# Kernel tuning notes

Hardware: AMD Instinct MI355X
Metric: run time of the kernel (lower is better)

The kernel has to match this reference:

```python
import jax, jax.numpy as jnp
import numpy as np

K = 3
PAD = 1


def conv2d(x, w, b, pad):
    y = jax.lax.conv_general_dilated(
        x, w, window_strides=(1, 1), padding=[(pad, pad), (pad, pad)],
        dimension_numbers=("NCHW", "OIHW", "NCHW"))
    return y + b[None, :, None, None]


def dcn_v2(f, w_off, b_off, w, b):
    # Modulated deformable conv (DCNv2), stride=1, pad=1, dilation=1, dg=1.
    B, C, H, W = f.shape
    om = conv2d(f, w_off, b_off, PAD)                 # [B, 27, H, W]
    o1, o2, m = jnp.split(om, 3, axis=1)
    offset = jnp.concatenate([o1, o2], axis=1).reshape(B, K * K, 2, H, W)
    dy, dx = offset[:, :, 0], offset[:, :, 1]          # [B, 9, H, W]
    mask = jax.nn.sigmoid(m)                           # [B, 9, H, W]
    ky = (jnp.arange(K * K) // K).astype(f.dtype)      # kernel row per tap
    kx = (jnp.arange(K * K) % K).astype(f.dtype)       # kernel col per tap
    hh = jnp.arange(H, dtype=f.dtype)
    ww = jnp.arange(W, dtype=f.dtype)
    ys = hh[None, None, :, None] - PAD + ky[None, :, None, None] + dy  # [B,9,H,W]
    xs = ww[None, None, None, :] - PAD + kx[None, :, None, None] + dx
    y0 = jnp.floor(ys)
    x0 = jnp.floor(xs)
    wy1 = ys - y0
    wx1 = xs - x0
    wy0 = 1.0 - wy1
    wx0 = 1.0 - wx1
    f_flat = f.reshape(B, C, H * W)

    def gather(yi, xi):
        valid = (yi >= 0) & (yi <= H - 1) & (xi >= 0) & (xi <= W - 1)
        yc = jnp.clip(yi, 0, H - 1).astype(jnp.int32)
        xc = jnp.clip(xi, 0, W - 1).astype(jnp.int32)
        idx = (yc * W + xc).reshape(B, 1, -1)          # [B,1,9*H*W]
        g = jnp.take_along_axis(f_flat, idx, axis=2).reshape(B, C, K * K, H, W)
        return g * valid.astype(f.dtype).reshape(B, 1, K * K, H, W)

    v = (gather(y0, x0) * (wy0 * wx0)[:, None]
         + gather(y0, x0 + 1) * (wy0 * wx1)[:, None]
         + gather(y0 + 1, x0) * (wy1 * wx0)[:, None]
         + gather(y0 + 1, x0 + 1) * (wy1 * wx1)[:, None])   # [B,C,9,H,W]
    v = v * mask[:, None]
    out = jnp.einsum("bckhw,ock->bohw", v, w.reshape(w.shape[0], C, K * K))
    return out + b[None, :, None, None]


def setup_inputs() -> dict:
    key = jax.random.key(0)
    ks = jax.random.split(key, 10)
    B, C, H, W = 2, 256, 128, 128
    s = 0.05
    return {
        "x": jax.random.normal(ks[0], (B, C, H, W), jnp.float32),
        "votes": jax.random.normal(ks[1], (B, C, H, W), jnp.float32),
        "w1": jax.random.normal(ks[2], (C, C, 3, 3), jnp.float32) * s,
        "b1": jnp.zeros((C,), jnp.float32),
        "w_off": jax.random.normal(ks[3], (27, C, 3, 3), jnp.float32) * 0.01,
        "b_off": jnp.zeros((27,), jnp.float32),
        "w_dcn": jax.random.normal(ks[4], (C, C, 3, 3), jnp.float32) * s,
        "b_dcn": jnp.zeros((C,), jnp.float32),
        "w2": jax.random.normal(ks[5], (C, C, 3, 3), jnp.float32) * s,
        "b2": jnp.zeros((C,), jnp.float32),
        "w3": jax.random.normal(ks[6], (C, C, 3, 3), jnp.float32) * s,
        "b3": jnp.zeros((C,), jnp.float32),
        "w4": jax.random.normal(ks[7], (2, C, 1, 1), jnp.float32) * s,
        "b4": jnp.zeros((2,), jnp.float32),
    }


def reference(x, votes, w1, b1, w_off, b_off, w_dcn, b_dcn, w2, b2, w3, b3, w4, b4):
    v = jax.nn.relu(votes)
    t = jax.nn.relu(conv2d(v, w1, b1, PAD))            # conv3x3 + relu
    t = jax.nn.relu(dcn_v2(t, w_off, b_off, w_dcn, b_dcn))  # DCN + relu
    t = conv2d(t, w2, b2, PAD)                         # conv3x3 (no relu)
    g = t * x                                          # gated by x
    h = jax.nn.relu(conv2d(g, w3, b3, PAD))            # conv3x3 + relu
    out = conv2d(h, w4, b4, 0)                         # 1x1 -> outplanes
    return out
```

## Files before the change

### kernel.cpp

```cpp
#include <hip/hip_runtime.h>
#include <math.h>

typedef short short8 __attribute__((ext_vector_type(8)));
typedef float f32x4 __attribute__((ext_vector_type(4)));
typedef unsigned int uint4v __attribute__((ext_vector_type(4)));
typedef unsigned short ushort_t;

__device__ inline ushort_t f2bf(float f) {
    unsigned u = __builtin_bit_cast(unsigned, f);
    u = (u + 0x7fffu + ((u >> 16) & 1u)) >> 16;
    return (ushort_t)u;
}
__device__ inline float bf2f(ushort_t u) {
    return __builtin_bit_cast(float, (unsigned)u << 16);
}
__device__ inline void gload_lds16(const ushort_t* g, short* l) {
    __builtin_amdgcn_global_load_lds((const __attribute__((address_space(1))) unsigned int*)g,
                                     (__attribute__((address_space(3))) unsigned int*)l, 16, 0, 0);
}

__device__ inline void wpack_body(const float* __restrict__ w, ushort_t* __restrict__ wpk,
                                  int COUT, int NF, int bidLocal, int tid) {
    int T = bidLocal * 256 + tid;
    int lane = T & 63;
    int rest = T >> 6;
    int n = rest % NF;
    int kstep = rest / NF;
    int t = kstep >> 3, cc = kstep & 7;
    int oc = n * 16 + (lane & 15);
    int kk = (lane >> 4) * 8;
    short8 sv;
#pragma unroll
    for (int j = 0; j < 8; ++j) {
        int ci = cc * 32 + kk + j;
        float val = (oc < COUT) ? w[((size_t)oc * 256 + ci) * 9 + t] : 0.f;
        sv[j] = (short)f2bf(val);
    }
    *(short8*)&wpk[(size_t)T * 8] = sv;
}

__global__ __launch_bounds__(256)
void wpack_all_kernel(const float* w1, ushort_t* wpk1,
                      const float* w_off, ushort_t* wpkO,
                      const float* w_dcn, ushort_t* wpkD,
                      const float* w2, ushort_t* wpk2,
                      const float* w3, ushort_t* wpk3,
                      ushort_t* zp) {
    int bid = blockIdx.x, tid = threadIdx.x;
    if (bid < 288)       wpack_body(w1,    wpk1, 256, 16, bid,        tid);
    else if (bid < 324)  wpack_body(w_off, wpkO, 27,  2,  bid - 288,  tid);
    else if (bid < 612)  wpack_body(w_dcn, wpkD, 256, 16, bid - 324,  tid);
    else if (bid < 900)  wpack_body(w2,    wpk2, 256, 16, bid - 612,  tid);
    else if (bid < 1188) wpack_body(w3,    wpk3, 256, 16, bid - 900,  tid);
    else                 zp[tid] = 0;
}

__global__ __launch_bounds__(256)
void nhwc_all_kernel(const float* __restrict__ votes, const float* __restrict__ x,
                     ushort_t* __restrict__ aN, ushort_t* __restrict__ xN) {
    __shared__ short s[64 * 66];
    const int tid = threadIdx.x;
    const int px0 = blockIdx.x * 64;
    const int ci0 = blockIdx.y * 64;
    const int z   = blockIdx.z;
    const int b   = z & 1;
    const bool doRelu = (z < 2);
    const float* inb = (doRelu ? votes : x) + (size_t)b * 256 * 16384;
    ushort_t* ob = (doRelu ? aN : xN) + (size_t)b * 16384 * 256;
#pragma unroll
    for (int rep = 0; rep < 16; ++rep) {
        int cl = rep * 4 + (tid >> 6);
        int pl = tid & 63;
        float v = inb[(size_t)(ci0 + cl) * 16384 + px0 + pl];
        if (doRelu) v = fmaxf(v, 0.f);
        s[pl * 66 + cl] = (short)f2bf(v);
    }
    __syncthreads();
#pragma unroll
    for (int rep = 0; rep < 2; ++rep) {
        int c = rep * 256 + tid;
        int pl = c >> 3;
        int cl = (c & 7) * 8;
        *(short8*)&ob[(size_t)(px0 + pl) * 256 + ci0 + cl] = *(const short8*)&s[pl * 66 + cl];
    }
}

template<int TW, int OUTC, int EPI>
__global__ __launch_bounds__(512, 2)
void conv_mfma_kernel(const ushort_t* __restrict__ in, const ushort_t* __restrict__ wpk,
                      const float* __restrict__ bias, int coutReal,
                      const ushort_t* __restrict__ xin, ushort_t* __restrict__ outp,
                      const ushort_t* __restrict__ zp)
{
    constexpr int NF = OUTC / 16;
    constexpr int NN = (NF < 4) ? NF : 4;
    constexpr int HWD = TW + 2;
    constexpr int HPX = 6 * HWD;
    constexpr int ROUNDS = (HPX * 4 + 511) / 512;
    constexpr int MW  = TW / 16;
    constexpr int MPW = TW / 8;
    constexpr int PITCH = OUTC + 4;
    union SM { short a[2][ROUNDS * 512 * 8]; float e[TW * PITCH]; };
    __shared__ __align__(16) SM sm;

    const int tid  = threadIdx.x;
    const int lane = tid & 63;
    const int wv   = tid >> 6;
    const int hi   = lane >> 4;
    const int lo   = lane & 15;
    const int pxg  = wv & 1;
    const int wn   = wv >> 1;
    const int wnu  = __builtin_amdgcn_readfirstlane(wn);
    const int x0 = blockIdx.x * TW;
    const int y0 = blockIdx.y * 4;
    const int b  = blockIdx.z;
    const ushort_t* inb = in + (size_t)b * 16384 * 256;

    const ushort_t* sptr[ROUNDS];
    int sstep[ROUNDS];
#pragma unroll
    for (int r = 0; r < ROUNDS; ++r) {
        int g = r * 512 + tid;
        int px = g >> 2, slot = g & 3;
        int hy = px / HWD, hx = px - hy * HWD;
        int gy = y0 - 1 + hy, gx = x0 - 1 + hx;
        bool ok = (px < HPX) && ((unsigned)gy < 128u) && ((unsigned)gx < 128u);
        int kk = (px ^ (px >> 2)) & 3;
        sptr[r] = ok ? (inb + (size_t)((gy << 7) + gx) * 256 + ((slot ^ kk) << 3))
                     : (zp + (slot << 3));
        sstep[r] = ok ? 32 : 0;
    }

    int pxh_base[MPW];
#pragma unroll
    for (int m = 0; m < MPW; ++m)
        pxh_base[m] = (2 * pxg + m / MW) * HWD + (m % MW) * 16 + lo;

    f32x4 acc[MPW][NN];
#pragma unroll
    for (int m = 0; m < MPW; ++m)
#pragma unroll
        for (int n = 0; n < NN; ++n) acc[m][n] = (f32x4){0.f, 0.f, 0.f, 0.f};

#pragma unroll
    for (int r = 0; r < ROUNDS; ++r)
        gload_lds16(sptr[r], &sm.a[0][(r * 512 + wv * 64) * 8]);
    __syncthreads();

    for (int cc = 0; cc < 8; ++cc) {
        const int buf = cc & 1;
        if (cc < 7) {
#pragma unroll
            for (int r = 0; r < ROUNDS; ++r)
                gload_lds16(sptr[r] + (size_t)(cc + 1) * sstep[r],
                            &sm.a[buf ^ 1][(r * 512 + wv * 64) * 8]);
        }
        if (NF >= 4 || wnu == 0) {
#pragma unroll
            for (int t = 0; t < 9; ++t) {
                const int ky = t / 3, kx = t % 3;
                short8 bf[NN];
#pragma unroll
                for (int n = 0; n < NN; ++n)
                    bf[n] = *(const short8*)&wpk[((size_t)((t * 8 + cc) * NF + wnu * NN + n) * 64 + lane) * 8];
                short8 af[MPW];
#pragma unroll
                for (int m = 0; m < MPW; ++m) {
                    int ph = pxh_base[m] + ky * HWD + kx;
                    int off = ph * 32 + ((hi ^ ((ph ^ (ph >> 2)) & 3)) << 3);
                    af[m] = *(const short8*)&sm.a[buf][off];
                }
#pragma unroll
                for (int m = 0; m < MPW; ++m)
#pragma unroll
                    for (int n = 0; n < NN; ++n)
                        acc[m][n] = __builtin_amdgcn_mfma_f32_16x16x32_bf16(af[m], bf[n], acc[m][n], 0, 0, 0);
            }
        }
        __syncthreads();
    }

    float br[NN];
#pragma unroll
    for (int n = 0; n < NN; ++n) {
        int oc = wn * (16 * NN) + n * 16 + lo;
        br[n] = (oc < coutReal) ? bias[oc] : 0.f;
    }
    const size_t obase = ((size_t)b * 16384 + (size_t)y0 * 128 + x0) * OUTC;
#pragma unroll
    for (int p = 0; p < 4; ++p) {
        if (pxg == (p >> 1) && (NF >= 4 || wnu == 0)) {
#pragma unroll
            for (int mm = 0; mm < MW; ++mm) {
                int m = (p & 1) * MW + mm;
#pragma unroll
                for (int n = 0; n < NN; ++n)
#pragma unroll
                    for (int r = 0; r < 4; ++r) {
                        int col = mm * 16 + hi * 4 + r;
                        float v = acc[m][n][r] + br[n];
                        if (EPI == 1) v = fmaxf(v, 0.f);
                        sm.e[col * PITCH + wn * (16 * NN) + n * 16 + lo] = v;
                    }
            }
        }
        __syncthreads();
        constexpr int CHUNKS = TW * OUTC / 8;
        for (int c = tid; c < CHUNKS; c += 512) {
            int col = c / (OUTC / 8);
            int ch = c % (OUTC / 8);
            f32x4 v0 = *(const f32x4*)&sm.e[col * PITCH + ch * 8];
            f32x4 v1 = *(const f32x4*)&sm.e[col * PITCH + ch * 8 + 4];
            size_t gidx = obase + ((size_t)p * 128 + col) * OUTC + ch * 8;
            if (EPI == 2) {
                uint4v xu = *(const uint4v*)&xin[gidx];
#pragma unroll
                for (int j = 0; j < 4; ++j) {
                    float xa = bf2f((ushort_t)(xu[j] & 0xffffu));
                    float xb = __builtin_bit_cast(float, xu[j] & 0xffff0000u);
                    if (j < 2) { v0[2 * j] *= xa; v0[2 * j + 1] *= xb; }
                    else       { v1[2 * (j - 2)] *= xa; v1[2 * (j - 2) + 1] *= xb; }
                }
            }
            short8 s;
#pragma unroll
            for (int j = 0; j < 4; ++j) s[j] = (short)f2bf(v0[j]);
#pragma unroll
            for (int j = 0; j < 4; ++j) s[4 + j] = (short)f2bf(v1[j]);
            *(short8*)&outp[gidx] = s;
        }
        __syncthreads();
    }
}

__device__ inline void corner8(uint4v u, float w, float* sv) {
#pragma unroll
    for (int j = 0; j < 4; ++j) {
        unsigned a = u[j];
        sv[2 * j]     = fmaf(w, __builtin_bit_cast(float, a << 16), sv[2 * j]);
        sv[2 * j + 1] = fmaf(w, __builtin_bit_cast(float, a & 0xffff0000u), sv[2 * j + 1]);
    }
}

__global__ __launch_bounds__(256, 2)
void dcn_mfma_kernel(const ushort_t* __restrict__ ft, const ushort_t* __restrict__ omt,
                     const ushort_t* __restrict__ wpk, const float* __restrict__ bias,
                     ushort_t* __restrict__ outp)
{
    union SM { short a[2][2][2048]; float e[16 * 264]; };
    __shared__ __align__(16) SM sm;

    const int tid  = threadIdx.x;
    const int lane = tid & 63;
    const int wv   = tid >> 6;
    const int hi   = lane >> 4;
    const int lo   = lane & 15;
    const int bid  = blockIdx.x;
    const int tile = (bid & 7) * 64 + (bid >> 3);
    const int b    = tile >> 8;
    const int rem  = tile & 255;
    const int y0   = (rem >> 3) * 4;
    const int x0   = (rem & 7) * 16;
    const ushort_t* fb = ft + (size_t)b * 16384 * 256;

    const int pxl = (wv << 4) | (lane >> 2);
    const int q   = lane & 3;

    float mw[9][4];
    unsigned mc[9];
    {
        const int py = y0 + (pxl >> 4), pxx = x0 + (pxl & 15);
        const ushort_t* omp = omt + ((size_t)b * 16384 + py * 128 + pxx) * 32;
        uint4v ow[4];
#pragma unroll
        for (int j = 0; j < 4; ++j) ow[j] = *(const uint4v*)(omp + j * 8);
        unsigned wbuf[14];
#pragma unroll
        for (int j = 0; j < 4; ++j)
#pragma unroll
            for (int e = 0; e < 4; ++e)
                if (j * 4 + e < 14) wbuf[j * 4 + e] = ow[j][e];
#pragma unroll
        for (int t = 0; t < 9; ++t) {
            float dy = bf2f((ushort_t)(wbuf[t] & 0xffffu));
            float dx = bf2f((ushort_t)(wbuf[t] >> 16));
            unsigned mw_ = wbuf[(18 + t) >> 1];
            float mr = ((18 + t) & 1) ? bf2f((ushort_t)(mw_ >> 16)) : bf2f((ushort_t)(mw_ & 0xffffu));
            float mk = 1.f / (1.f + expf(-mr));
            float ys = (float)(py - 1 + t / 3) + dy;
            float xs = (float)(pxx - 1 + t % 3) + dx;
            float y0f = floorf(ys), x0f = floorf(xs);
            float wy1 = ys - y0f, wx1 = xs - x0f;
            float wy0 = 1.f - wy1, wx0 = 1.f - wx1;
            int yi = (int)y0f, xi = (int)x0f;
            bool vy0 = (yi >= 0) && (yi < 128), vy1 = (yi + 1 >= 0) && (yi + 1 < 128);
            bool vx0 = (xi >= 0) && (xi < 128), vx1 = (xi + 1 >= 0) && (xi + 1 < 128);
            mw[t][0] = (vy0 && vx0) ? wy0 * wx0 * mk : 0.f;
            mw[t][1] = (vy0 && vx1) ? wy0 * wx1 * mk : 0.f;
            mw[t][2] = (vy1 && vx0) ? wy1 * wx0 * mk : 0.f;
            mw[t][3] = (vy1 && vx1) ? wy1 * wx1 * mk : 0.f;
            int y0c = min(max(yi, 0), 127), y1c = min(max(yi + 1, 0), 127);
            int x0c = min(max(xi, 0), 127), x1c = min(max(xi + 1, 0), 127);
            mc[t] = (unsigned)y0c | ((unsigned)y1c << 8) | ((unsigned)x0c << 16) | ((unsigned)x1c << 24);
        }
    }

    const int w_off = pxl * 32 + ((q ^ ((pxl ^ (pxl >> 2)) & 3)) << 3);
    int a_off[4];
#pragma unroll
    for (int m = 0; m < 4; ++m) {
        int p_ = m * 16 + lo;
        a_off[m] = p_ * 32 + ((hi ^ ((p_ ^ (p_ >> 2)) & 3)) << 3);
    }

    f32x4 acc[4][4];
#pragma unroll
    for (int m = 0; m < 4; ++m)
#pragma unroll
        for (int n = 0; n < 4; ++n) acc[m][n] = (f32x4){0.f, 0.f, 0.f, 0.f};

    uint4v n0a, n0b, n0c, n0d;
    uint4v n1a, n1b, n1c, n1d;

    {
        unsigned c = mc[0];
        int yy0 = c & 255, yy1 = (c >> 8) & 255, xx0 = (c >> 16) & 255, xx1 = c >> 24;
        size_t o00 = (size_t)((yy0 << 7) + xx0) * 256, o01 = (size_t)((yy0 << 7) + xx1) * 256;
        size_t o10 = (size_t)((yy1 << 7) + xx0) * 256, o11 = (size_t)((yy1 << 7) + xx1) * 256;
#pragma unroll
        for (int h = 0; h < 2; ++h) {
            const ushort_t* pc = fb + h * 32 + q * 8;
            uint4v g0 = *(const uint4v*)(pc + o00);
            uint4v g1 = *(const uint4v*)(pc + o01);
            uint4v g2 = *(const uint4v*)(pc + o10);
            uint4v g3 = *(const uint4v*)(pc + o11);
            float sv[8] = {0.f, 0.f, 0.f, 0.f, 0.f, 0.f, 0.f, 0.f};
            corner8(g0, mw[0][0], sv); corner8(g1, mw[0][1], sv);
            corner8(g2, mw[0][2], sv); corner8(g3, mw[0][3], sv);
            unsigned pk[4];
#pragma unroll
            for (int j = 0; j < 4; ++j)
                asm("v_cvt_pk_bf16_f32 %0, %1, %2" : "=v"(pk[j]) : "v"(sv[2 * j]), "v"(sv[2 * j + 1]));
            *(uint4v*)&sm.a[0][h][w_off] = (uint4v){pk[0], pk[1], pk[2], pk[3]};
        }
    }
    __syncthreads();

    for (int cch = 0; cch < 4; ++cch) {
#pragma unroll
        for (int t = 0; t < 9; ++t) {
            const int cur = (cch + t) & 1;
            const bool last = (cch == 3) && (t == 8);
            const int tn   = (t == 8) ? 0 : t + 1;
            const int cchn = (t == 8) ? cch + 1 : cch;
            if (!last) {
                unsigned c = mc[tn];
                int yy0 = c & 255, yy1 = (c >> 8) & 255, xx0 = (c >> 16) & 255, xx1 = c >> 24;
                size_t o00 = (size_t)((yy0 << 7) + xx0) * 256, o01 = (size_t)((yy0 << 7) + xx1) * 256;
                size_t o10 = (size_t)((yy1 << 7) + xx0) * 256, o11 = (size_t)((yy1 << 7) + xx1) * 256;
                const ushort_t* pc0 = fb + (2 * cchn) * 32 + q * 8;
                n0a = *(const uint4v*)(pc0 + o00);
                n0b = *(const uint4v*)(pc0 + o01);
                n0c = *(const uint4v*)(pc0 + o10);
                n0d = *(const uint4v*)(pc0 + o11);
                const ushort_t* pc1 = pc0 + 32;
                n1a = *(const uint4v*)(pc1 + o00);
                n1b = *(const uint4v*)(pc1 + o01);
                n1c = *(const uint4v*)(pc1 + o10);
                n1d = *(const uint4v*)(pc1 + o11);
            }
            short8 bfr0[4], bfr1[4];
            {
                const ushort_t* bs0 = wpk + ((size_t)((t * 8 + 2 * cch) * 16 + wv * 4) * 64 + lane) * 8;
#pragma unroll
                for (int n = 0; n < 4; ++n)
                    bfr0[n] = *(const short8*)(bs0 + (size_t)n * 512);
                const ushort_t* bs1 = bs0 + 16 * 512;
#pragma unroll
                for (int n = 0; n < 4; ++n)
                    bfr1[n] = *(const short8*)(bs1 + (size_t)n * 512);
            }
#pragma unroll
            for (int m = 0; m < 4; ++m) {
                short8 af0 = *(const short8*)&sm.a[cur][0][a_off[m]];
                short8 af1 = *(const short8*)&sm.a[cur][1][a_off[m]];
#pragma unroll
                for (int n = 0; n < 4; ++n)
                    acc[m][n] = __builtin_amdgcn_mfma_f32_16x16x32_bf16(af0, bfr0[n], acc[m][n], 0, 0, 0);
#pragma unroll
                for (int n = 0; n < 4; ++n)
                    acc[m][n] = __builtin_amdgcn_mfma_f32_16x16x32_bf16(af1, bfr1[n], acc[m][n], 0, 0, 0);
            }
            if (!last) {
                {
                    float sv[8] = {0.f, 0.f, 0.f, 0.f, 0.f, 0.f, 0.f, 0.f};
                    corner8(n0a, mw[tn][0], sv); corner8(n0b, mw[tn][1], sv);
                    corner8(n0c, mw[tn][2], sv); corner8(n0d, mw[tn][3], sv);
                    unsigned pk[4];
#pragma unroll
                    for (int j = 0; j < 4; ++j)
                        asm("v_cvt_pk_bf16_f32 %0, %1, %2" : "=v"(pk[j]) : "v"(sv[2 * j]), "v"(sv[2 * j + 1]));
                    *(uint4v*)&sm.a[cur ^ 1][0][w_off] = (uint4v){pk[0], pk[1], pk[2], pk[3]};
                }
                {
                    float sv[8] = {0.f, 0.f, 0.f, 0.f, 0.f, 0.f, 0.f, 0.f};
                    corner8(n1a, mw[tn][0], sv); corner8(n1b, mw[tn][1], sv);
                    corner8(n1c, mw[tn][2], sv); corner8(n1d, mw[tn][3], sv);
                    unsigned pk[4];
#pragma unroll
                    for (int j = 0; j < 4; ++j)
                        asm("v_cvt_pk_bf16_f32 %0, %1, %2" : "=v"(pk[j]) : "v"(sv[2 * j]), "v"(sv[2 * j + 1]));
                    *(uint4v*)&sm.a[cur ^ 1][1][w_off] = (uint4v){pk[0], pk[1], pk[2], pk[3]};
                }
            }
            __syncthreads();
        }
    }

    float br[4];
#pragma unroll
    for (int n = 0; n < 4; ++n) br[n] = bias[wv * 64 + n * 16 + lo];
#pragma unroll
    for (int p = 0; p < 4; ++p) {
#pragma unroll
        for (int n = 0; n < 4; ++n)
#pragma unroll
            for (int r = 0; r < 4; ++r)
                sm.e[(hi * 4 + r) * 264 + wv * 64 + n * 16 + lo] = fmaxf(acc[p][n][r] + br[n], 0.f);
        __syncthreads();
#pragma unroll
        for (int j = 0; j < 2; ++j) {
            int c2 = j * 256 + tid;
            int pl = c2 >> 5, ch = c2 & 31;
            f32x4 v0 = *(const f32x4*)&sm.e[pl * 264 + ch * 8];
            f32x4 v1 = *(const f32x4*)&sm.e[pl * 264 + ch * 8 + 4];
            short8 s;
#pragma unroll
            for (int jj = 0; jj < 4; ++jj) s[jj] = (short)f2bf(v0[jj]);
#pragma unroll
            for (int jj = 0; jj < 4; ++jj) s[4 + jj] = (short)f2bf(v1[jj]);
            *(short8*)&outp[((size_t)b * 16384 + (size_t)(y0 + p) * 128 + x0 + pl) * 256 + ch * 8] = s;
        }
        __syncthreads();
    }
}

__global__ __launch_bounds__(256)
void conv1x1_kernel(const ushort_t* __restrict__ in, const float* __restrict__ w,
                    const float* __restrict__ bias, float* __restrict__ out)
{
    __shared__ float sw[512];
    for (int i = threadIdx.x; i < 512; i += 256) sw[i] = w[i];
    __syncthreads();
    int px = blockIdx.x * 256 + threadIdx.x;
    int b = px >> 14, p = px & 16383;
    const ushort_t* ip = in + (size_t)px * 256;
    float a0 = 0.f, a1 = 0.f;
#pragma unroll
    for (int ch = 0; ch < 32; ++ch) {
        uint4v u = *(const uint4v*)&ip[ch * 8];
#pragma unroll
        for (int j = 0; j < 4; ++j) {
            int ci = ch * 8 + 2 * j;
            float fa = __builtin_bit_cast(float, u[j] << 16);
            float fb = __builtin_bit_cast(float, u[j] & 0xffff0000u);
            a0 = fmaf(fa, sw[ci], a0);      a1 = fmaf(fa, sw[256 + ci], a1);
            a0 = fmaf(fb, sw[ci + 1], a0);  a1 = fmaf(fb, sw[256 + ci + 1], a1);
        }
    }
    out[(size_t)b * 2 * 16384 + p]         = a0 + bias[0];
    out[(size_t)b * 2 * 16384 + 16384 + p] = a1 + bias[1];
}

extern "C" void kernel_launch(void* const* d_in, const int* in_sizes, int n_in,
                              void* d_out, int out_size, void* d_ws, size_t ws_size,
                              hipStream_t stream) {
    const float* x     = (const float*)d_in[0];
    const float* votes = (const float*)d_in[1];
    const float* w1    = (const float*)d_in[2];
    const float* b1    = (const float*)d_in[3];
    const float* w_off = (const float*)d_in[4];
    const float* b_off = (const float*)d_in[5];
    const float* w_dcn = (const float*)d_in[6];
    const float* b_dcn = (const float*)d_in[7];
    const float* w2    = (const float*)d_in[8];
    const float* b2    = (const float*)d_in[9];
    const float* w3    = (const float*)d_in[10];
    const float* b3    = (const float*)d_in[11];
    const float* w4    = (const float*)d_in[12];
    const float* b4    = (const float*)d_in[13];
    float* outp = (float*)d_out;

    const int B = 2;
    const size_t featN = (size_t)B * 16384 * 256;

    ushort_t* ws   = (ushort_t*)d_ws;
    ushort_t* t1   = ws;
    ushort_t* t2   = t1 + featN;
    ushort_t* aN   = t2 + featN;
    ushort_t* xN   = aN + featN;
    ushort_t* om   = xN + featN;
    ushort_t* wpk1 = om + (size_t)B * 16384 * 32;
    ushort_t* wpkO = wpk1 + 589824;
    ushort_t* wpkD = wpkO + 73728;
    ushort_t* wpk2 = wpkD + 589824;
    ushort_t* wpk3 = wpk2 + 589824;
    ushort_t* zp   = wpk3 + 589824;

    wpack_all_kernel<<<1189, 256, 0, stream>>>(w1, wpk1, w_off, wpkO, w_dcn, wpkD,
                                               w2, wpk2, w3, wpk3, zp);
    nhwc_all_kernel<<<dim3(256, 4, 4), 256, 0, stream>>>(votes, x, aN, xN);

    dim3 cg16(8, 32, B);
    dim3 cg32(4, 32, B);
    conv_mfma_kernel<16, 256, 1><<<cg16, 512, 0, stream>>>(aN, wpk1, b1, 256, nullptr, t1, zp);
    conv_mfma_kernel<32, 32, 0><<<cg32, 512, 0, stream>>>(t1, wpkO, b_off, 27, nullptr, om, zp);
    dcn_mfma_kernel<<<512, 256, 0, stream>>>(t1, om, wpkD, b_dcn, t2);
    conv_mfma_kernel<16, 256, 2><<<cg16, 512, 0, stream>>>(t2, wpk2, b2, 256, xN, aN, zp);
    conv_mfma_kernel<16, 256, 1><<<cg16, 512, 0, stream>>>(aN, wpk3, b3, 256, nullptr, xN, zp);
    conv1x1_kernel<<<128, 256, 0, stream>>>(xN, w4, b4, outp);
}
```

Before: 259.8 us.

## Fuse 1x1 head conv into final conv epilogue; double-buffer DCN weight loads

The final 3x3 conv gets a new epilogue that applies ReLU, dot-products each pixel's 256 channels with the two 1x1 output filters, reduces across 32 lanes with shuffles, and writes fp32 output directly. This drops the bf16 intermediate write/read and the separate conv1x1 launch. Separately, the DCN kernel's main loop is unrolled by two so B-fragment weight loads for the next tap are issued into alternate register sets before the current MFMAs. That overlaps weight-load latency but increases register pressure.

```diff
diff --git a/kernel.cpp b/kernel.cpp
--- a/kernel.cpp
+++ b/kernel.cpp
@@ -90,7 +90,9 @@
 void conv_mfma_kernel(const ushort_t* __restrict__ in, const ushort_t* __restrict__ wpk,
                       const float* __restrict__ bias, int coutReal,
                       const ushort_t* __restrict__ xin, ushort_t* __restrict__ outp,
-                      const ushort_t* __restrict__ zp)
+                      const ushort_t* __restrict__ zp,
+                      const float* __restrict__ w4g, const float* __restrict__ b4g,
+                      float* __restrict__ out4)
 {
     constexpr int NF = OUTC / 16;
     constexpr int NN = (NF < 4) ? NF : 4;
@@ -199,35 +201,60 @@
                     for (int r = 0; r < 4; ++r) {
                         int col = mm * 16 + hi * 4 + r;
                         float v = acc[m][n][r] + br[n];
-                        if (EPI == 1) v = fmaxf(v, 0.f);
+                        if (EPI == 1 || EPI == 3) v = fmaxf(v, 0.f);
                         sm.e[col * PITCH + wn * (16 * NN) + n * 16 + lo] = v;
                     }
             }
         }
         __syncthreads();
-        constexpr int CHUNKS = TW * OUTC / 8;
-        for (int c = tid; c < CHUNKS; c += 512) {
-            int col = c / (OUTC / 8);
-            int ch = c % (OUTC / 8);
+        if constexpr (EPI == 3) {
+            int col = tid >> 5;
+            int ch  = tid & 31;
             f32x4 v0 = *(const f32x4*)&sm.e[col * PITCH + ch * 8];
             f32x4 v1 = *(const f32x4*)&sm.e[col * PITCH + ch * 8 + 4];
-            size_t gidx = obase + ((size_t)p * 128 + col) * OUTC + ch * 8;
-            if (EPI == 2) {
-                uint4v xu = *(const uint4v*)&xin[gidx];
-#pragma unroll
-                for (int j = 0; j < 4; ++j) {
-                    float xa = bf2f((ushort_t)(xu[j] & 0xffffu));
-                    float xb = __builtin_bit_cast(float, xu[j] & 0xffff0000u);
-                    if (j < 2) { v0[2 * j] *= xa; v0[2 * j + 1] *= xb; }
-                    else       { v1[2 * (j - 2)] *= xa; v1[2 * (j - 2) + 1] *= xb; }
+            float4 wa0 = *(const float4*)&w4g[ch * 8];
+            float4 wa1 = *(const float4*)&w4g[ch * 8 + 4];
+            float4 wb0 = *(const float4*)&w4g[256 + ch * 8];
+            float4 wb1 = *(const float4*)&w4g[256 + ch * 8 + 4];
+            float a0 = v0[0] * wa0.x + v0[1] * wa0.y + v0[2] * wa0.z + v0[3] * wa0.w
+                     + v1[0] * wa1.x + v1[1] * wa1.y + v1[2] * wa1.z + v1[3] * wa1.w;
+            float a1 = v0[0] * wb0.x + v0[1] * wb0.y + v0[2] * wb0.z + v0[3] * wb0.w
+                     + v1[0] * wb1.x + v1[1] * wb1.y + v1[2] * wb1.z + v1[3] * wb1.w;
+#pragma unroll
+            for (int s = 16; s >= 1; s >>= 1) {
+                a0 += __shfl_xor(a0, s);
+                a1 += __shfl_xor(a1, s);
+            }
+            if (ch == 0) {
+                size_t o = (size_t)b * 2 * 16384 + (size_t)(y0 + p) * 128 + x0 + col;
+                out4[o]         = a0 + b4g[0];
+                out4[o + 16384] = a1 + b4g[1];
+            }
+        } else {
+            constexpr int CHUNKS = TW * OUTC / 8;
+            for (int c = tid; c < CHUNKS; c += 512) {
+                int col = c / (OUTC / 8);
+                int ch = c % (OUTC / 8);
+                f32x4 v0 = *(const f32x4*)&sm.e[col * PITCH + ch * 8];
+                f32x4 v1 = *(const f32x4*)&sm.e[col * PITCH + ch * 8 + 4];
+                size_t gidx = obase + ((size_t)p * 128 + col) * OUTC + ch * 8;
+                if (EPI == 2) {
+                    uint4v xu = *(const uint4v*)&xin[gidx];
+#pragma unroll
+                    for (int j = 0; j < 4; ++j) {
+                        float xa = bf2f((ushort_t)(xu[j] & 0xffffu));
+                        float xb = __builtin_bit_cast(float, xu[j] & 0xffff0000u);
+                        if (j < 2) { v0[2 * j] *= xa; v0[2 * j + 1] *= xb; }
+                        else       { v1[2 * (j - 2)] *= xa; v1[2 * (j - 2) + 1] *= xb; }
+                    }
                 }
-            }
-            short8 s;
-#pragma unroll
-            for (int j = 0; j < 4; ++j) s[j] = (short)f2bf(v0[j]);
-#pragma unroll
-            for (int j = 0; j < 4; ++j) s[4 + j] = (short)f2bf(v1[j]);
-            *(short8*)&outp[gidx] = s;
+                short8 s;
+#pragma unroll
+                for (int j = 0; j < 4; ++j) s[j] = (short)f2bf(v0[j]);
+#pragma unroll
+                for (int j = 0; j < 4; ++j) s[4 + j] = (short)f2bf(v1[j]);
+                *(short8*)&outp[gidx] = s;
+            }
         }
         __syncthreads();
     }
@@ -241,6 +268,27 @@
         sv[2 * j + 1] = fmaf(w, __builtin_bit_cast(float, a & 0xffff0000u), sv[2 * j + 1]);
     }
 }
+
+#define DCN_LOADB(D0, D1, T_, CCH_) { \
+    const ushort_t* bs = wpk + ((size_t)(((T_) * 8 + 2 * (CCH_)) * 16 + wv * 4) * 64 + lane) * 8; \
+    _Pragma("unroll") \
+    for (int n = 0; n < 4; ++n) { \
+        D0[n] = *(const short8*)(bs + (size_t)n * 512); \
+        D1[n] = *(const short8*)(bs + (size_t)(16 + n) * 512); \
+    } }
+
+#define DCN_MFMA(B0, B1, CUR) { \
+    _Pragma("unroll") \
+    for (int m = 0; m < 4; ++m) { \
+        short8 af0 = *(const short8*)&sm.a[CUR][0][a_off[m]]; \
+        short8 af1 = *(const short8*)&sm.a[CUR][1][a_off[m]]; \
+        _Pragma("unroll") \
+        for (int n = 0; n < 4; ++n) \
+            acc[m][n] = __builtin_amdgcn_mfma_f32_16x16x32_bf16(af0, B0[n], acc[m][n], 0, 0, 0); \
+        _Pragma("unroll") \
+        for (int n = 0; n < 4; ++n) \
+            acc[m][n] = __builtin_amdgcn_mfma_f32_16x16x32_bf16(af1, B1[n], acc[m][n], 0, 0, 0); \
+    } }
 
 __global__ __launch_bounds__(256, 2)
 void dcn_mfma_kernel(const ushort_t* __restrict__ ft, const ushort_t* __restrict__ omt,
@@ -321,6 +369,7 @@
 
     uint4v n0a, n0b, n0c, n0d;
     uint4v n1a, n1b, n1c, n1d;
+    short8 bA0[4], bA1[4], bB0[4], bB1[4];
 
     {
         unsigned c = mc[0];
@@ -343,14 +392,17 @@
                 asm("v_cvt_pk_bf16_f32 %0, %1, %2" : "=v"(pk[j]) : "v"(sv[2 * j]), "v"(sv[2 * j + 1]));
             *(uint4v*)&sm.a[0][h][w_off] = (uint4v){pk[0], pk[1], pk[2], pk[3]};
         }
+        DCN_LOADB(bA0, bA1, 0, 0);
     }
     __syncthreads();
 
-    for (int cch = 0; cch < 4; ++cch) {
-#pragma unroll
-        for (int t = 0; t < 9; ++t) {
-            const int cur = (cch + t) & 1;
-            const bool last = (cch == 3) && (t == 8);
+    for (int cch2 = 0; cch2 < 2; ++cch2) {
+#pragma unroll
+        for (int kk = 0; kk < 18; ++kk) {
+            const int t   = (kk < 9) ? kk : kk - 9;
+            const int cch = 2 * cch2 + ((kk >= 9) ? 1 : 0);
+            const int cur = kk & 1;
+            const bool last = (cch2 == 1) && (kk == 17);
             const int tn   = (t == 8) ? 0 : t + 1;
             const int cchn = (t == 8) ? cch + 1 : cch;
             if (!last) {
@@ -369,27 +421,12 @@
                 n1c = *(const uint4v*)(pc1 + o10);
                 n1d = *(const uint4v*)(pc1 + o11);
             }
-            short8 bfr0[4], bfr1[4];
-            {
-                const ushort_t* bs0 = wpk + ((size_t)((t * 8 + 2 * cch) * 16 + wv * 4) * 64 + lane) * 8;
-#pragma unroll
-                for (int n = 0; n < 4; ++n)
-                    bfr0[n] = *(const short8*)(bs0 + (size_t)n * 512);
-                const ushort_t* bs1 = bs0 + 16 * 512;
-#pragma unroll
-                for (int n = 0; n < 4; ++n)
-                    bfr1[n] = *(const short8*)(bs1 + (size_t)n * 512);
-            }
-#pragma unroll
-            for (int m = 0; m < 4; ++m) {
-                short8 af0 = *(const short8*)&sm.a[cur][0][a_off[m]];
-                short8 af1 = *(const short8*)&sm.a[cur][1][a_off[m]];
-#pragma unroll
-                for (int n = 0; n < 4; ++n)
-                    acc[m][n] = __builtin_amdgcn_mfma_f32_16x16x32_bf16(af0, bfr0[n], acc[m][n], 0, 0, 0);
-#pragma unroll
-                for (int n = 0; n < 4; ++n)
-                    acc[m][n] = __builtin_amdgcn_mfma_f32_16x16x32_bf16(af1, bfr1[n], acc[m][n], 0, 0, 0);
+            if (cur == 0) {
+                if (!last) DCN_LOADB(bB0, bB1, tn, cchn);
+                DCN_MFMA(bA0, bA1, 0);
+            } else {
+                if (!last) DCN_LOADB(bA0, bA1, tn, cchn);
+                DCN_MFMA(bB0, bB1, 1);
             }
             if (!last) {
                 {
@@ -443,33 +480,6 @@
         }
         __syncthreads();
     }
-}
-
-__global__ __launch_bounds__(256)
-void conv1x1_kernel(const ushort_t* __restrict__ in, const float* __restrict__ w,
-                    const float* __restrict__ bias, float* __restrict__ out)
-{
-    __shared__ float sw[512];
-    for (int i = threadIdx.x; i < 512; i += 256) sw[i] = w[i];
-    __syncthreads();
-    int px = blockIdx.x * 256 + threadIdx.x;
-    int b = px >> 14, p = px & 16383;
-    const ushort_t* ip = in + (size_t)px * 256;
-    float a0 = 0.f, a1 = 0.f;
-#pragma unroll
-    for (int ch = 0; ch < 32; ++ch) {
-        uint4v u = *(const uint4v*)&ip[ch * 8];
-#pragma unroll
-        for (int j = 0; j < 4; ++j) {
-            int ci = ch * 8 + 2 * j;
-            float fa = __builtin_bit_cast(float, u[j] << 16);
-            float fb = __builtin_bit_cast(float, u[j] & 0xffff0000u);
-            a0 = fmaf(fa, sw[ci], a0);      a1 = fmaf(fa, sw[256 + ci], a1);
-            a0 = fmaf(fb, sw[ci + 1], a0);  a1 = fmaf(fb, sw[256 + ci + 1], a1);
-        }
-    }
-    out[(size_t)b * 2 * 16384 + p]         = a0 + bias[0];
-    out[(size_t)b * 2 * 16384 + 16384 + p] = a1 + bias[1];
 }
 
 extern "C" void kernel_launch(void* const* d_in, const int* in_sizes, int n_in,
@@ -513,10 +523,9 @@
 
     dim3 cg16(8, 32, B);
     dim3 cg32(4, 32, B);
-    conv_mfma_kernel<16, 256, 1><<<cg16, 512, 0, stream>>>(aN, wpk1, b1, 256, nullptr, t1, zp);
-    conv_mfma_kernel<32, 32, 0><<<cg32, 512, 0, stream>>>(t1, wpkO, b_off, 27, nullptr, om, zp);
+    conv_mfma_kernel<16, 256, 1><<<cg16, 512, 0, stream>>>(aN, wpk1, b1, 256, nullptr, t1, zp, nullptr, nullptr, nullptr);
+    conv_mfma_kernel<32, 32, 0><<<cg32, 512, 0, stream>>>(t1, wpkO, b_off, 27, nullptr, om, zp, nullptr, nullptr, nullptr);
     dcn_mfma_kernel<<<512, 256, 0, stream>>>(t1, om, wpkD, b_dcn, t2);
-    conv_mfma_kernel<16, 256, 2><<<cg16, 512, 0, stream>>>(t2, wpk2, b2, 256, xN, aN, zp);
-    conv_mfma_kernel<16, 256, 1><<<cg16, 512, 0, stream>>>(aN, wpk3, b3, 256, nullptr, xN, zp);
-    conv1x1_kernel<<<128, 256, 0, stream>>>(xN, w4, b4, outp);
-}
+    conv_mfma_kernel<16, 256, 2><<<cg16, 512, 0, stream>>>(t2, wpk2, b2, 256, xN, aN, zp, nullptr, nullptr, nullptr);
+    conv_mfma_kernel<16, 256, 3><<<cg16, 512, 0, stream>>>(aN, wpk3, b3, 256, nullptr, nullptr, zp, w4, b4, outp);
+}
```

Measured after the change: 265.1 us. 2.1% more time.
